# Kernel optimization log

Measured on AMD Instinct MI355X. Metric: run time of the kernel, lower is better.

## Reference

```python
import jax, jax.numpy as jnp
import numpy as np

N = 50000          # num nodes
E = 800000         # num edges (avg degree 16)
IN_C, HID_C, OUT_C = 128, 128, 64
LPA_ITER = 5


def setup_inputs() -> dict:
    key = jax.random.key(0)
    ks = jax.random.split(key, 8)
    x = jax.random.normal(ks[0], (N, IN_C), dtype=jnp.float32)
    soft_labels = jax.random.uniform(ks[1], (N, OUT_C), dtype=jnp.float32)
    edge_index = jax.random.randint(ks[2], (2, E), 0, N, dtype=jnp.int64)
    # learnable edge weights: abs() in the original, so keep them positive
    edge_attr = jax.random.uniform(ks[3], (E,), dtype=jnp.float32, minval=0.1, maxval=1.0)
    # GCNConv params (lin weight + bias)
    w1 = jax.random.normal(ks[4], (IN_C, HID_C), dtype=jnp.float32) / np.sqrt(IN_C)
    b1 = jnp.zeros((HID_C,), dtype=jnp.float32)
    w2 = jax.random.normal(ks[5], (HID_C, OUT_C), dtype=jnp.float32) / np.sqrt(HID_C)
    b2 = jnp.zeros((OUT_C,), dtype=jnp.float32)
    return {"x": x, "soft_labels": soft_labels, "edge_attr": edge_attr,
            "w1": w1, "b1": b1, "w2": w2, "b2": b2, "edge_index": edge_index}


def reference(x, soft_labels, edge_attr, w1, b1, w2, b2, edge_index):
    row, col = edge_index[0], edge_index[1]
    n = x.shape[0]
    # row-normalize the weighted sparse adjacency: A_n = D^{-1} A
    deg = jax.ops.segment_sum(edge_attr, row, num_segments=n)  # [N]
    deg_inv = jnp.where(deg == 0, 0.0, 1.0 / deg)              # inf -> 0
    val = deg_inv[row] * edge_attr                              # [E]

    def spmm(v):  # A_n @ v,  v: [N, F]
        return jax.ops.segment_sum(val[:, None] * v[col], row, num_segments=n)

    # eval mode: dropout(p=0.5, training=False) is identity
    h = jax.nn.relu(spmm(x @ w1) + b1)        # GCNConv 1 (normalize=False)
    logits = spmm(h @ w2) + b2                # GCNConv 2
    x_out = jax.nn.sigmoid(logits)

    labels = soft_labels
    for _ in range(LPA_ITER):                 # label propagation
        labels = spmm(labels)
    labels = jax.nn.sigmoid(labels)
    return (x_out, labels)
```

## Files before the change

kernel.cpp:

```cpp
#include <hip/hip_runtime.h>
#include <cstdint>
#include <cstddef>


#define WS_ALIGN(x) (((x) + 255) & ~((size_t)255))

typedef __attribute__((ext_vector_type(8))) short short8;
typedef __attribute__((ext_vector_type(4))) float floatx4;

__device__ __forceinline__ unsigned short f2bf(float f) {
    unsigned u = __float_as_uint(f);
    u += 0x7fffu + ((u >> 16) & 1u);
    return (unsigned short)(u >> 16);
}
__device__ __forceinline__ float bf2f(unsigned short h) {
    return __uint_as_float(((unsigned)h) << 16);
}
__device__ __forceinline__ float sigmoidf(float x) {
    return 1.f / (1.f + __expf(-x));
}

static const int NBLK = 256;
#define MAXNB 256

__launch_bounds__(256)
__global__ void binA_count(const int* __restrict__ row, int* __restrict__ bucket_count,
                           int* __restrict__ bases, int E, int chunk, int NB)
{
    __shared__ int hist[MAXNB];
    const int t = threadIdx.x;
    const int blk = blockIdx.x;
    if (t < NB) hist[t] = 0;
    __syncthreads();
    const int s = blk * chunk;
    const int e = min(E, s + chunk);
    for (int i = s + t; i < e; i += 256)
        atomicAdd(&hist[row[i] >> 8], 1);
    __syncthreads();
    if (t < NB)
        bases[blk * NB + t] = atomicAdd(&bucket_count[t], hist[t]);
}

__launch_bounds__(256)
__global__ void bin_scan(const int* __restrict__ bucket_count, int* __restrict__ bucket_start,
                         int NB)
{
    __shared__ int s[256];
    const int t = threadIdx.x;
    int v = (t < NB) ? bucket_count[t] : 0;
    s[t] = v;
    __syncthreads();
    for (int off = 1; off < 256; off <<= 1) {
        int u = (t >= off) ? s[t - off] : 0;
        __syncthreads();
        s[t] += u;
        __syncthreads();
    }
    int excl = s[t] - v;
    if (t <= NB) bucket_start[t] = excl;
}

__launch_bounds__(256)
__global__ void binA_scatter(const int* __restrict__ row, const int* __restrict__ colv,
                             const float* __restrict__ ea,
                             const int* __restrict__ bucket_start, const int* __restrict__ bases,
                             int2* __restrict__ bk, int E, int chunk, int NB)
{
    __shared__ int cur[MAXNB];
    const int t = threadIdx.x;
    const int blk = blockIdx.x;
    if (t < NB) cur[t] = bucket_start[t] + bases[blk * NB + t];
    __syncthreads();
    const int s = blk * chunk;
    const int e = min(E, s + chunk);
    for (int i = s + t; i < e; i += 256) {
        int r = row[i];
        int bin = r >> 8;
        int pos = atomicAdd(&cur[bin], 1);
        bk[pos] = make_int2(((r & 255) << 16) | colv[i], __float_as_int(ea[i]));
    }
}

__launch_bounds__(256)
__global__ void binB(const int2* __restrict__ bk, const int* __restrict__ bucket_start,
                     int* __restrict__ rowptr, int2* __restrict__ edges, int N)
{
    __shared__ int cnt[256];
    __shared__ float deg[256];
    __shared__ float inv[256];
    __shared__ int excl_s[256];
    __shared__ int cur[256];
    __shared__ int scantmp[256];
    const int b = blockIdx.x;
    const int t = threadIdx.x;
    const int s = bucket_start[b];
    const int e = bucket_start[b + 1];
    cnt[t] = 0;
    deg[t] = 0.f;
    __syncthreads();
    for (int i = s + t; i < e; i += 256) {
        int2 v = bk[i];
        int rl = ((unsigned)v.x) >> 16;
        atomicAdd(&cnt[rl], 1);
        atomicAdd(&deg[rl], __int_as_float(v.y));
    }
    __syncthreads();
    const int myc = cnt[t];
    scantmp[t] = myc;
    __syncthreads();
    for (int off = 1; off < 256; off <<= 1) {
        int u = (t >= off) ? scantmp[t - off] : 0;
        __syncthreads();
        scantmp[t] += u;
        __syncthreads();
    }
    const int excl = scantmp[t] - myc;
    excl_s[t] = excl;
    float d = deg[t];
    inv[t] = (d > 0.f) ? 1.f / d : 0.f;
    cur[t] = 0;
    const int gr = b * 256 + t;
    if (gr <= N) rowptr[gr] = s + excl;
    __syncthreads();
    for (int i = s + t; i < e; i += 256) {
        int2 v = bk[i];
        int rl = ((unsigned)v.x) >> 16;
        int c = v.x & 0xffff;
        int p = s + excl_s[rl] + atomicAdd(&cur[rl], 1);
        edges[p] = make_int2(c, __float_as_int(__int_as_float(v.y) * inv[rl]));
    }
}

__global__ void f32_to_bf16_kernel(const float* __restrict__ in, unsigned short* __restrict__ out,
                                   int n2)
{
    int i = blockIdx.x * 256 + threadIdx.x;
    if (i < n2) {
        float2 v = ((const float2*)in)[i];
        unsigned p = (unsigned)f2bf(v.x) | ((unsigned)f2bf(v.y) << 16);
        ((unsigned*)out)[i] = p;
    }
}

template<int COLS>
__global__ void pack_w_kernel(const float* __restrict__ W, unsigned short* __restrict__ Wp)
{
    const int total = (COLS / 16) * 4 * 64;
    int idx = blockIdx.x * 256 + threadIdx.x;
    if (idx >= total) return;
    const int l = idx & 63;
    const int t = (idx >> 6) & 3;
    const int ct = idx >> 8;
    const int kbase = t * 32 + (l >> 4) * 8;
    const int col = ct * 16 + (l & 15);
    unsigned short v[8];
#pragma unroll
    for (int j = 0; j < 8; ++j)
        v[j] = f2bf(W[(size_t)(kbase + j) * COLS + col]);
    uint4 o;
    o.x = (unsigned)v[0] | ((unsigned)v[1] << 16);
    o.y = (unsigned)v[2] | ((unsigned)v[3] << 16);
    o.z = (unsigned)v[4] | ((unsigned)v[5] << 16);
    o.w = (unsigned)v[6] | ((unsigned)v[7] << 16);
    *(uint4*)(Wp + (size_t)idx * 8) = o;
}

template<int COLS>
__launch_bounds__(256)
__global__ void gemm_mfma_f32a(const float* __restrict__ A,
                               const unsigned short* __restrict__ Wp,
                               unsigned short* __restrict__ C, int M)
{
    const int wave = threadIdx.x >> 6;
    const int lane = threadIdx.x & 63;
    const int row0 = blockIdx.x * 64 + wave * 16;
    const int m = lane & 15;
    const int q = lane >> 4;

    const int arow = row0 + m;
    const bool avalid = arow < M;
    short8 a[4];
#pragma unroll
    for (int t = 0; t < 4; ++t) {
        if (avalid) {
            float4 f0 = *(const float4*)(A + (size_t)arow * 128 + t * 32 + q * 8);
            float4 f1 = *(const float4*)(A + (size_t)arow * 128 + t * 32 + q * 8 + 4);
            a[t][0] = (short)f2bf(f0.x); a[t][1] = (short)f2bf(f0.y);
            a[t][2] = (short)f2bf(f0.z); a[t][3] = (short)f2bf(f0.w);
            a[t][4] = (short)f2bf(f1.x); a[t][5] = (short)f2bf(f1.y);
            a[t][6] = (short)f2bf(f1.z); a[t][7] = (short)f2bf(f1.w);
        } else {
            a[t] = (short8)0;
        }
    }

#pragma unroll
    for (int ct = 0; ct < COLS / 16; ++ct) {
        floatx4 acc = {0.f, 0.f, 0.f, 0.f};
#pragma unroll
        for (int t = 0; t < 4; ++t) {
            short8 b = *(const short8*)(Wp + (size_t)((ct * 4 + t) * 64 + lane) * 8);
            acc = __builtin_amdgcn_mfma_f32_16x16x32_bf16(a[t], b, acc, 0, 0, 0);
        }
        const int col = ct * 16 + m;
#pragma unroll
        for (int r = 0; r < 4; ++r) {
            int orow = row0 + q * 4 + r;
            if (orow < M)
                C[(size_t)orow * COLS + col] = f2bf(acc[r]);
        }
    }
}

template<int COLS>
__launch_bounds__(256)
__global__ void gemm_mfma(const unsigned short* __restrict__ A,
                          const unsigned short* __restrict__ Wp,
                          unsigned short* __restrict__ C, int M)
{
    const int wave = threadIdx.x >> 6;
    const int lane = threadIdx.x & 63;
    const int row0 = blockIdx.x * 64 + wave * 16;
    const int m = lane & 15;
    const int q = lane >> 4;

    const int arow = row0 + m;
    const bool avalid = arow < M;
    short8 a[4];
#pragma unroll
    for (int t = 0; t < 4; ++t) {
        if (avalid)
            a[t] = *(const short8*)(A + (size_t)arow * 128 + t * 32 + q * 8);
        else
            a[t] = (short8)0;
    }

#pragma unroll
    for (int ct = 0; ct < COLS / 16; ++ct) {
        floatx4 acc = {0.f, 0.f, 0.f, 0.f};
#pragma unroll
        for (int t = 0; t < 4; ++t) {
            short8 b = *(const short8*)(Wp + (size_t)((ct * 4 + t) * 64 + lane) * 8);
            acc = __builtin_amdgcn_mfma_f32_16x16x32_bf16(a[t], b, acc, 0, 0, 0);
        }
        const int col = ct * 16 + m;
#pragma unroll
        for (int r = 0; r < 4; ++r) {
            int orow = row0 + q * 4 + r;
            if (orow < M)
                C[(size_t)orow * COLS + col] = f2bf(acc[r]);
        }
    }
}

__launch_bounds__(256)
__global__ void spmm_f128_f64(const int* __restrict__ rowptr, const int2* __restrict__ edges,
                              const unsigned* __restrict__ srcA,
                              const unsigned short* __restrict__ srcB,
                              const float* __restrict__ bias,
                              unsigned* __restrict__ outA,
                              unsigned short* __restrict__ outB,
                              int n)
{
    const int row = blockIdx.x * 4 + (threadIdx.x >> 6);
    const int lane = threadIdx.x & 63;
    if (row >= n) return;
    const int s = rowptr[row];
    const int e = rowptr[row + 1];

    float ax[8], ay[8], ab[8];
#pragma unroll
    for (int j = 0; j < 8; ++j) { ax[j] = 0.f; ay[j] = 0.f; ab[j] = 0.f; }
    int i = s;
    for (; i + 8 <= e; i += 8) {
        int2 ed[8];
        unsigned ua[8];
        unsigned short ub[8];
#pragma unroll
        for (int j = 0; j < 8; ++j) ed[j] = edges[i + j];
#pragma unroll
        for (int j = 0; j < 8; ++j) ua[j] = srcA[(size_t)ed[j].x * 64 + lane];
#pragma unroll
        for (int j = 0; j < 8; ++j) ub[j] = srcB[(size_t)ed[j].x * 64 + lane];
#pragma unroll
        for (int j = 0; j < 8; ++j) {
            float w = __int_as_float(ed[j].y);
            ax[j] = fmaf(w, __uint_as_float(ua[j] << 16), ax[j]);
            ay[j] = fmaf(w, __uint_as_float(ua[j] & 0xffff0000u), ay[j]);
            ab[j] = fmaf(w, bf2f(ub[j]), ab[j]);
        }
    }
    for (; i < e; ++i) {
        int2 e0 = edges[i];
        unsigned ua = srcA[(size_t)e0.x * 64 + lane];
        unsigned short ub = srcB[(size_t)e0.x * 64 + lane];
        float w = __int_as_float(e0.y);
        ax[0] = fmaf(w, __uint_as_float(ua << 16), ax[0]);
        ay[0] = fmaf(w, __uint_as_float(ua & 0xffff0000u), ay[0]);
        ab[0] = fmaf(w, bf2f(ub), ab[0]);
    }
    float vx = ((ax[0] + ax[1]) + (ax[2] + ax[3])) + ((ax[4] + ax[5]) + (ax[6] + ax[7]));
    float vy = ((ay[0] + ay[1]) + (ay[2] + ay[3])) + ((ay[4] + ay[5]) + (ay[6] + ay[7]));
    float vb = ((ab[0] + ab[1]) + (ab[2] + ab[3])) + ((ab[4] + ab[5]) + (ab[6] + ab[7]));
    float2 b = *(const float2*)(bias + lane * 2);
    vx = fmaxf(vx + b.x, 0.f);
    vy = fmaxf(vy + b.y, 0.f);
    outA[(size_t)row * 64 + lane] = (unsigned)f2bf(vx) | ((unsigned)f2bf(vy) << 16);
    outB[(size_t)row * 64 + lane] = f2bf(vb);
}

__launch_bounds__(256)
__global__ void spmm_f64_f64(const int* __restrict__ rowptr, const int2* __restrict__ edges,
                             const unsigned short* __restrict__ srcA,
                             const unsigned short* __restrict__ srcB,
                             const float* __restrict__ bias,
                             float* __restrict__ outA,
                             unsigned short* __restrict__ outB,
                             int n)
{
    const int row = blockIdx.x * 4 + (threadIdx.x >> 6);
    const int lane = threadIdx.x & 63;
    if (row >= n) return;
    const int s = rowptr[row];
    const int e = rowptr[row + 1];

    float aa[8], ab[8];
#pragma unroll
    for (int j = 0; j < 8; ++j) { aa[j] = 0.f; ab[j] = 0.f; }
    int i = s;
    for (; i + 8 <= e; i += 8) {
        int2 ed[8];
        unsigned short ua[8], ub[8];
#pragma unroll
        for (int j = 0; j < 8; ++j) ed[j] = edges[i + j];
#pragma unroll
        for (int j = 0; j < 8; ++j) ua[j] = srcA[(size_t)ed[j].x * 64 + lane];
#pragma unroll
        for (int j = 0; j < 8; ++j) ub[j] = srcB[(size_t)ed[j].x * 64 + lane];
#pragma unroll
        for (int j = 0; j < 8; ++j) {
            float w = __int_as_float(ed[j].y);
            aa[j] = fmaf(w, bf2f(ua[j]), aa[j]);
            ab[j] = fmaf(w, bf2f(ub[j]), ab[j]);
        }
    }
    for (; i < e; ++i) {
        int2 e0 = edges[i];
        float w = __int_as_float(e0.y);
        aa[0] = fmaf(w, bf2f(srcA[(size_t)e0.x * 64 + lane]), aa[0]);
        ab[0] = fmaf(w, bf2f(srcB[(size_t)e0.x * 64 + lane]), ab[0]);
    }
    float va = ((aa[0] + aa[1]) + (aa[2] + aa[3])) + ((aa[4] + aa[5]) + (aa[6] + aa[7]));
    float vb = ((ab[0] + ab[1]) + (ab[2] + ab[3])) + ((ab[4] + ab[5]) + (ab[6] + ab[7]));
    outA[(size_t)row * 64 + lane] = sigmoidf(va + bias[lane]);
    outB[(size_t)row * 64 + lane] = f2bf(vb);
}

template<int ACT, bool OUT_BF16>
__launch_bounds__(256)
__global__ void spmm64_kernel(const int* __restrict__ rowptr, const int2* __restrict__ edges,
                              const unsigned short* __restrict__ src,
                              void* __restrict__ out, int n)
{
    const int row = blockIdx.x * 4 + (threadIdx.x >> 6);
    const int lane = threadIdx.x & 63;
    if (row >= n) return;
    const int s = rowptr[row];
    const int e = rowptr[row + 1];

    float a[8];
#pragma unroll
    for (int j = 0; j < 8; ++j) a[j] = 0.f;
    int i = s;
    for (; i + 8 <= e; i += 8) {
        int2 ed[8];
        float sv[8];
#pragma unroll
        for (int j = 0; j < 8; ++j) ed[j] = edges[i + j];
#pragma unroll
        for (int j = 0; j < 8; ++j) sv[j] = bf2f(src[(size_t)ed[j].x * 64 + lane]);
#pragma unroll
        for (int j = 0; j < 8; ++j) a[j] = fmaf(__int_as_float(ed[j].y), sv[j], a[j]);
    }
    for (; i < e; ++i) {
        int2 e0 = edges[i];
        a[0] = fmaf(__int_as_float(e0.y), bf2f(src[(size_t)e0.x * 64 + lane]), a[0]);
    }
    float v = ((a[0] + a[1]) + (a[2] + a[3])) + ((a[4] + a[5]) + (a[6] + a[7]));
    if (ACT == 3) v = sigmoidf(v);
    if (OUT_BF16)
        ((unsigned short*)out)[(size_t)row * 64 + lane] = f2bf(v);
    else
        ((float*)out)[(size_t)row * 64 + lane] = v;
}

extern "C" void kernel_launch(void* const* d_in, const int* in_sizes, int n_in,
                              void* d_out, int out_size, void* d_ws, size_t ws_size,
                              hipStream_t stream)
{
    const float* x    = (const float*)d_in[0];
    const float* soft = (const float*)d_in[1];
    const float* ea   = (const float*)d_in[2];
    const float* w1   = (const float*)d_in[3];
    const float* b1   = (const float*)d_in[4];
    const float* w2   = (const float*)d_in[5];
    const float* b2   = (const float*)d_in[6];
    const int*   eidx = (const int*)d_in[7];

    const int N = in_sizes[0] / 128;
    const int E = in_sizes[2];
    const int* row  = eidx;
    const int* colv = eidx + E;
    const int NB = (N + 255) / 256;
    const int chunk = (E + NBLK - 1) / NBLK;

    uint8_t* ws = (uint8_t*)d_ws;
    size_t off = 0;
    auto alloc = [&](size_t bytes) -> void* {
        void* p = ws + off;
        off += WS_ALIGN(bytes);
        return p;
    };
    int*  bucket_count = (int*) alloc((size_t)NB * 4);
    int*  bucket_start = (int*) alloc(((size_t)NB + 1) * 4);
    int*  bases        = (int*) alloc((size_t)NBLK * NB * 4);
    int*  rowptr       = (int*) alloc(((size_t)N + 1) * 4);
    int2* bk           = (int2*)alloc((size_t)E * 8);
    int2* edges        = (int2*)alloc((size_t)E * 8);
    unsigned short* w1p     = (unsigned short*)alloc((size_t)128 * 128 * 2);
    unsigned short* w2p     = (unsigned short*)alloc((size_t)128 * 64 * 2);
    unsigned short* xw1b    = (unsigned short*)alloc((size_t)N * 128 * 2);
    unsigned short* hb      = (unsigned short*)alloc((size_t)N * 128 * 2);
    unsigned short* logitsb = (unsigned short*)alloc((size_t)N * 64 * 2);
    unsigned short* softb   = (unsigned short*)alloc((size_t)N * 64 * 2);
    unsigned short* labA    = (unsigned short*)alloc((size_t)N * 64 * 2);
    unsigned short* labB    = (unsigned short*)alloc((size_t)N * 64 * 2);

    float* out0 = (float*)d_out;
    float* out1 = out0 + (size_t)N * 64;

    hipMemsetAsync(bucket_count, 0, (size_t)NB * 4, stream);

    binA_count<<<NBLK, 256, 0, stream>>>(row, bucket_count, bases, E, chunk, NB);
    bin_scan<<<1, 256, 0, stream>>>(bucket_count, bucket_start, NB);
    binA_scatter<<<NBLK, 256, 0, stream>>>(row, colv, ea, bucket_start, bases, bk, E, chunk, NB);
    binB<<<NB, 256, 0, stream>>>(bk, bucket_start, rowptr, edges, N);

    const int ns2 = (N * 64) / 2;
    f32_to_bf16_kernel<<<(ns2 + 255) / 256, 256, 0, stream>>>(soft, softb, ns2);
    pack_w_kernel<128><<<8, 256, 0, stream>>>(w1, w1p);
    pack_w_kernel<64><<<4, 256, 0, stream>>>(w2, w2p);

    const int gGemm = (N + 63) / 64;
    const int gSp   = (N + 3) / 4;

    gemm_mfma_f32a<128><<<gGemm, 256, 0, stream>>>(x, w1p, xw1b, N);

    spmm_f128_f64<<<gSp, 256, 0, stream>>>(rowptr, edges, (const unsigned*)xw1b, softb,
                                           b1, (unsigned*)hb, labA, N);

    gemm_mfma<64><<<gGemm, 256, 0, stream>>>(hb, w2p, logitsb, N);

    spmm_f64_f64<<<gSp, 256, 0, stream>>>(rowptr, edges, logitsb, labA, b2, out0, labB, N);

    spmm64_kernel<0, true ><<<gSp, 256, 0, stream>>>(rowptr, edges, labB, labA, N);
    spmm64_kernel<0, true ><<<gSp, 256, 0, stream>>>(rowptr, edges, labA, labB, N);
    spmm64_kernel<3, false><<<gSp, 256, 0, stream>>>(rowptr, edges, labB, out1, N);
}
```

Baseline: 361.9 us.

## Split each SpMM row across four edge-quarters with vectorized bf16 gathers, merge small kernels

The SpMM kernels now assign each wave's four 16-lane quarters to different edges. Each lane gathers a vector (uint2/uint4) of packed bf16 features, and the partial sums are combined with cross-lane shuffles at the end. Edge records are read with nontemporal loads. The bucket scan is folded into the scatter and binB kernels, and the weight and label conversions are merged into one prep kernel, which removes several launches. This widens memory transactions and increases edge-level parallelism, at the cost of redundant scans per block and idle lanes on low-degree rows.

```diff
diff --git a/kernel.cpp b/kernel.cpp
--- a/kernel.cpp
+++ b/kernel.cpp
@@ -13,11 +13,20 @@
     u += 0x7fffu + ((u >> 16) & 1u);
     return (unsigned short)(u >> 16);
 }
-__device__ __forceinline__ float bf2f(unsigned short h) {
-    return __uint_as_float(((unsigned)h) << 16);
+__device__ __forceinline__ float bf_lo(unsigned u) { return __uint_as_float(u << 16); }
+__device__ __forceinline__ float bf_hi(unsigned u) { return __uint_as_float(u & 0xffff0000u); }
+__device__ __forceinline__ unsigned pack_bf2(float a, float b) {
+    return (unsigned)f2bf(a) | ((unsigned)f2bf(b) << 16);
 }
 __device__ __forceinline__ float sigmoidf(float x) {
     return 1.f / (1.f + __expf(-x));
+}
+__device__ __forceinline__ int2 ld_nt_int2(const int2* p) {
+    long long v = __builtin_nontemporal_load((const long long*)p);
+    int2 r;
+    r.x = (int)(unsigned)(v & 0xffffffffLL);
+    r.y = (int)(v >> 32);
+    return r;
 }
 
 static const int NBLK = 256;
@@ -42,34 +51,25 @@
 }
 
 __launch_bounds__(256)
-__global__ void bin_scan(const int* __restrict__ bucket_count, int* __restrict__ bucket_start,
-                         int NB)
-{
-    __shared__ int s[256];
-    const int t = threadIdx.x;
-    int v = (t < NB) ? bucket_count[t] : 0;
-    s[t] = v;
-    __syncthreads();
-    for (int off = 1; off < 256; off <<= 1) {
-        int u = (t >= off) ? s[t - off] : 0;
-        __syncthreads();
-        s[t] += u;
-        __syncthreads();
-    }
-    int excl = s[t] - v;
-    if (t <= NB) bucket_start[t] = excl;
-}
-
-__launch_bounds__(256)
 __global__ void binA_scatter(const int* __restrict__ row, const int* __restrict__ colv,
                              const float* __restrict__ ea,
-                             const int* __restrict__ bucket_start, const int* __restrict__ bases,
+                             const int* __restrict__ bucket_count, const int* __restrict__ bases,
                              int2* __restrict__ bk, int E, int chunk, int NB)
 {
+    __shared__ int scan[256];
     __shared__ int cur[MAXNB];
     const int t = threadIdx.x;
     const int blk = blockIdx.x;
-    if (t < NB) cur[t] = bucket_start[t] + bases[blk * NB + t];
+    int v = (t < NB) ? bucket_count[t] : 0;
+    scan[t] = v;
+    __syncthreads();
+    for (int off = 1; off < 256; off <<= 1) {
+        int u = (t >= off) ? scan[t - off] : 0;
+        __syncthreads();
+        scan[t] += u;
+        __syncthreads();
+    }
+    if (t < NB) cur[t] = (scan[t] - v) + bases[blk * NB + t];
     __syncthreads();
     const int s = blk * chunk;
     const int e = min(E, s + chunk);
@@ -82,27 +82,39 @@
 }
 
 __launch_bounds__(256)
-__global__ void binB(const int2* __restrict__ bk, const int* __restrict__ bucket_start,
-                     int* __restrict__ rowptr, int2* __restrict__ edges, int N)
-{
+__global__ void binB(const int2* __restrict__ bk, const int* __restrict__ bucket_count,
+                     int* __restrict__ rowptr, int2* __restrict__ edges, int N, int NB)
+{
+    __shared__ int scan[256];
     __shared__ int cnt[256];
     __shared__ float deg[256];
     __shared__ float inv[256];
     __shared__ int excl_s[256];
     __shared__ int cur[256];
     __shared__ int scantmp[256];
+    __shared__ int sse[2];
     const int b = blockIdx.x;
     const int t = threadIdx.x;
-    const int s = bucket_start[b];
-    const int e = bucket_start[b + 1];
+    int v = (t < NB) ? bucket_count[t] : 0;
+    scan[t] = v;
+    __syncthreads();
+    for (int off = 1; off < 256; off <<= 1) {
+        int u = (t >= off) ? scan[t - off] : 0;
+        __syncthreads();
+        scan[t] += u;
+        __syncthreads();
+    }
+    if (t == b) { sse[0] = scan[t] - v; sse[1] = scan[t]; }
     cnt[t] = 0;
     deg[t] = 0.f;
     __syncthreads();
+    const int s = sse[0];
+    const int e = sse[1];
     for (int i = s + t; i < e; i += 256) {
-        int2 v = bk[i];
-        int rl = ((unsigned)v.x) >> 16;
+        int2 w = bk[i];
+        int rl = ((unsigned)w.x) >> 16;
         atomicAdd(&cnt[rl], 1);
-        atomicAdd(&deg[rl], __int_as_float(v.y));
+        atomicAdd(&deg[rl], __int_as_float(w.y));
     }
     __syncthreads();
     const int myc = cnt[t];
@@ -123,31 +135,18 @@
     if (gr <= N) rowptr[gr] = s + excl;
     __syncthreads();
     for (int i = s + t; i < e; i += 256) {
-        int2 v = bk[i];
-        int rl = ((unsigned)v.x) >> 16;
-        int c = v.x & 0xffff;
+        int2 w = bk[i];
+        int rl = ((unsigned)w.x) >> 16;
+        int c = w.x & 0xffff;
         int p = s + excl_s[rl] + atomicAdd(&cur[rl], 1);
-        edges[p] = make_int2(c, __float_as_int(__int_as_float(v.y) * inv[rl]));
-    }
-}
-
-__global__ void f32_to_bf16_kernel(const float* __restrict__ in, unsigned short* __restrict__ out,
-                                   int n2)
-{
-    int i = blockIdx.x * 256 + threadIdx.x;
-    if (i < n2) {
-        float2 v = ((const float2*)in)[i];
-        unsigned p = (unsigned)f2bf(v.x) | ((unsigned)f2bf(v.y) << 16);
-        ((unsigned*)out)[i] = p;
-    }
-}
-
-template<int COLS>
-__global__ void pack_w_kernel(const float* __restrict__ W, unsigned short* __restrict__ Wp)
-{
-    const int total = (COLS / 16) * 4 * 64;
-    int idx = blockIdx.x * 256 + threadIdx.x;
-    if (idx >= total) return;
+        edges[p] = make_int2(c, __float_as_int(__int_as_float(w.y) * inv[rl]));
+    }
+}
+
+__device__ __forceinline__ void pack_w_elem(const float* __restrict__ W,
+                                            unsigned short* __restrict__ Wp,
+                                            int idx, int COLS)
+{
     const int l = idx & 63;
     const int t = (idx >> 6) & 3;
     const int ct = idx >> 8;
@@ -163,6 +162,27 @@
     o.z = (unsigned)v[4] | ((unsigned)v[5] << 16);
     o.w = (unsigned)v[6] | ((unsigned)v[7] << 16);
     *(uint4*)(Wp + (size_t)idx * 8) = o;
+}
+
+__launch_bounds__(256)
+__global__ void prep_kernel(const float* __restrict__ w1, const float* __restrict__ w2,
+                            const float* __restrict__ soft,
+                            unsigned short* __restrict__ w1p, unsigned short* __restrict__ w2p,
+                            unsigned short* __restrict__ softb, int ns2)
+{
+    const int blk = blockIdx.x;
+    const int t = threadIdx.x;
+    if (blk < 8) {
+        pack_w_elem(w1, w1p, blk * 256 + t, 128);
+    } else if (blk < 12) {
+        pack_w_elem(w2, w2p, (blk - 8) * 256 + t, 64);
+    } else {
+        int i = (blk - 12) * 256 + t;
+        if (i < ns2) {
+            float2 v = ((const float2*)soft)[i];
+            ((unsigned*)softb)[i] = pack_bf2(v.x, v.y);
+        }
+    }
 }
 
 template<int COLS>
@@ -254,144 +274,246 @@
 }
 
 __launch_bounds__(256)
-__global__ void spmm_f128_f64(const int* __restrict__ rowptr, const int2* __restrict__ edges,
-                              const unsigned* __restrict__ srcA,
-                              const unsigned short* __restrict__ srcB,
-                              const float* __restrict__ bias,
-                              unsigned* __restrict__ outA,
-                              unsigned short* __restrict__ outB,
-                              int n)
+__global__ void fused1_quad(const int* __restrict__ rowptr, const int2* __restrict__ edges,
+                            const uint4* __restrict__ srcA,
+                            const uint2* __restrict__ srcB,
+                            const float* __restrict__ bias,
+                            uint4* __restrict__ outA,
+                            uint2* __restrict__ outB,
+                            int n)
 {
     const int row = blockIdx.x * 4 + (threadIdx.x >> 6);
     const int lane = threadIdx.x & 63;
+    const int fl = lane & 15;
+    const int q = lane >> 4;
     if (row >= n) return;
     const int s = rowptr[row];
     const int e = rowptr[row + 1];
 
-    float ax[8], ay[8], ab[8];
-#pragma unroll
-    for (int j = 0; j < 8; ++j) { ax[j] = 0.f; ay[j] = 0.f; ab[j] = 0.f; }
+    float ax[8], as[4];
+#pragma unroll
+    for (int j = 0; j < 8; ++j) ax[j] = 0.f;
+#pragma unroll
+    for (int j = 0; j < 4; ++j) as[j] = 0.f;
+
     int i = s;
-    for (; i + 8 <= e; i += 8) {
-        int2 ed[8];
-        unsigned ua[8];
-        unsigned short ub[8];
-#pragma unroll
-        for (int j = 0; j < 8; ++j) ed[j] = edges[i + j];
-#pragma unroll
-        for (int j = 0; j < 8; ++j) ua[j] = srcA[(size_t)ed[j].x * 64 + lane];
-#pragma unroll
-        for (int j = 0; j < 8; ++j) ub[j] = srcB[(size_t)ed[j].x * 64 + lane];
-#pragma unroll
-        for (int j = 0; j < 8; ++j) {
+    for (; i + 16 <= e; i += 16) {
+        int2 ed[4]; uint4 ua[4]; uint2 ub[4];
+#pragma unroll
+        for (int j = 0; j < 4; ++j) ed[j] = ld_nt_int2(&edges[i + 4 * j + q]);
+#pragma unroll
+        for (int j = 0; j < 4; ++j) ua[j] = srcA[(size_t)ed[j].x * 16 + fl];
+#pragma unroll
+        for (int j = 0; j < 4; ++j) ub[j] = srcB[(size_t)ed[j].x * 16 + fl];
+#pragma unroll
+        for (int j = 0; j < 4; ++j) {
             float w = __int_as_float(ed[j].y);
-            ax[j] = fmaf(w, __uint_as_float(ua[j] << 16), ax[j]);
-            ay[j] = fmaf(w, __uint_as_float(ua[j] & 0xffff0000u), ay[j]);
-            ab[j] = fmaf(w, bf2f(ub[j]), ab[j]);
-        }
-    }
-    for (; i < e; ++i) {
-        int2 e0 = edges[i];
-        unsigned ua = srcA[(size_t)e0.x * 64 + lane];
-        unsigned short ub = srcB[(size_t)e0.x * 64 + lane];
-        float w = __int_as_float(e0.y);
-        ax[0] = fmaf(w, __uint_as_float(ua << 16), ax[0]);
-        ay[0] = fmaf(w, __uint_as_float(ua & 0xffff0000u), ay[0]);
-        ab[0] = fmaf(w, bf2f(ub), ab[0]);
-    }
-    float vx = ((ax[0] + ax[1]) + (ax[2] + ax[3])) + ((ax[4] + ax[5]) + (ax[6] + ax[7]));
-    float vy = ((ay[0] + ay[1]) + (ay[2] + ay[3])) + ((ay[4] + ay[5]) + (ay[6] + ay[7]));
-    float vb = ((ab[0] + ab[1]) + (ab[2] + ab[3])) + ((ab[4] + ab[5]) + (ab[6] + ab[7]));
-    float2 b = *(const float2*)(bias + lane * 2);
-    vx = fmaxf(vx + b.x, 0.f);
-    vy = fmaxf(vy + b.y, 0.f);
-    outA[(size_t)row * 64 + lane] = (unsigned)f2bf(vx) | ((unsigned)f2bf(vy) << 16);
-    outB[(size_t)row * 64 + lane] = f2bf(vb);
-}
-
-__launch_bounds__(256)
-__global__ void spmm_f64_f64(const int* __restrict__ rowptr, const int2* __restrict__ edges,
-                             const unsigned short* __restrict__ srcA,
-                             const unsigned short* __restrict__ srcB,
-                             const float* __restrict__ bias,
-                             float* __restrict__ outA,
-                             unsigned short* __restrict__ outB,
-                             int n)
+            ax[0] = fmaf(w, bf_lo(ua[j].x), ax[0]); ax[1] = fmaf(w, bf_hi(ua[j].x), ax[1]);
+            ax[2] = fmaf(w, bf_lo(ua[j].y), ax[2]); ax[3] = fmaf(w, bf_hi(ua[j].y), ax[3]);
+            ax[4] = fmaf(w, bf_lo(ua[j].z), ax[4]); ax[5] = fmaf(w, bf_hi(ua[j].z), ax[5]);
+            ax[6] = fmaf(w, bf_lo(ua[j].w), ax[6]); ax[7] = fmaf(w, bf_hi(ua[j].w), ax[7]);
+            as[0] = fmaf(w, bf_lo(ub[j].x), as[0]); as[1] = fmaf(w, bf_hi(ub[j].x), as[1]);
+            as[2] = fmaf(w, bf_lo(ub[j].y), as[2]); as[3] = fmaf(w, bf_hi(ub[j].y), as[3]);
+        }
+    }
+    for (; i + 4 <= e; i += 4) {
+        int2 ed = ld_nt_int2(&edges[i + q]);
+        uint4 ua = srcA[(size_t)ed.x * 16 + fl];
+        uint2 ub = srcB[(size_t)ed.x * 16 + fl];
+        float w = __int_as_float(ed.y);
+        ax[0] = fmaf(w, bf_lo(ua.x), ax[0]); ax[1] = fmaf(w, bf_hi(ua.x), ax[1]);
+        ax[2] = fmaf(w, bf_lo(ua.y), ax[2]); ax[3] = fmaf(w, bf_hi(ua.y), ax[3]);
+        ax[4] = fmaf(w, bf_lo(ua.z), ax[4]); ax[5] = fmaf(w, bf_hi(ua.z), ax[5]);
+        ax[6] = fmaf(w, bf_lo(ua.w), ax[6]); ax[7] = fmaf(w, bf_hi(ua.w), ax[7]);
+        as[0] = fmaf(w, bf_lo(ub.x), as[0]); as[1] = fmaf(w, bf_hi(ub.x), as[1]);
+        as[2] = fmaf(w, bf_lo(ub.y), as[2]); as[3] = fmaf(w, bf_hi(ub.y), as[3]);
+    }
+    const int r = e - i;
+    if (q < r) {
+        int2 ed = ld_nt_int2(&edges[i + q]);
+        uint4 ua = srcA[(size_t)ed.x * 16 + fl];
+        uint2 ub = srcB[(size_t)ed.x * 16 + fl];
+        float w = __int_as_float(ed.y);
+        ax[0] = fmaf(w, bf_lo(ua.x), ax[0]); ax[1] = fmaf(w, bf_hi(ua.x), ax[1]);
+        ax[2] = fmaf(w, bf_lo(ua.y), ax[2]); ax[3] = fmaf(w, bf_hi(ua.y), ax[3]);
+        ax[4] = fmaf(w, bf_lo(ua.z), ax[4]); ax[5] = fmaf(w, bf_hi(ua.z), ax[5]);
+        ax[6] = fmaf(w, bf_lo(ua.w), ax[6]); ax[7] = fmaf(w, bf_hi(ua.w), ax[7]);
+        as[0] = fmaf(w, bf_lo(ub.x), as[0]); as[1] = fmaf(w, bf_hi(ub.x), as[1]);
+        as[2] = fmaf(w, bf_lo(ub.y), as[2]); as[3] = fmaf(w, bf_hi(ub.y), as[3]);
+    }
+#pragma unroll
+    for (int j = 0; j < 8; ++j) {
+        ax[j] += __shfl_down(ax[j], 32);
+        ax[j] += __shfl_down(ax[j], 16);
+    }
+#pragma unroll
+    for (int j = 0; j < 4; ++j) {
+        as[j] += __shfl_down(as[j], 32);
+        as[j] += __shfl_down(as[j], 16);
+    }
+    if (q == 0) {
+        float4 b0 = *(const float4*)(bias + 8 * fl);
+        float4 b1 = *(const float4*)(bias + 8 * fl + 4);
+        float h0 = fmaxf(ax[0] + b0.x, 0.f), h1 = fmaxf(ax[1] + b0.y, 0.f);
+        float h2 = fmaxf(ax[2] + b0.z, 0.f), h3 = fmaxf(ax[3] + b0.w, 0.f);
+        float h4 = fmaxf(ax[4] + b1.x, 0.f), h5 = fmaxf(ax[5] + b1.y, 0.f);
+        float h6 = fmaxf(ax[6] + b1.z, 0.f), h7 = fmaxf(ax[7] + b1.w, 0.f);
+        uint4 oa;
+        oa.x = pack_bf2(h0, h1); oa.y = pack_bf2(h2, h3);
+        oa.z = pack_bf2(h4, h5); oa.w = pack_bf2(h6, h7);
+        outA[(size_t)row * 16 + fl] = oa;
+        uint2 ob;
+        ob.x = pack_bf2(as[0], as[1]);
+        ob.y = pack_bf2(as[2], as[3]);
+        outB[(size_t)row * 16 + fl] = ob;
+    }
+}
+
+__launch_bounds__(256)
+__global__ void fused2_quad(const int* __restrict__ rowptr, const int2* __restrict__ edges,
+                            const uint2* __restrict__ srcA,
+                            const uint2* __restrict__ srcB,
+                            const float* __restrict__ bias,
+                            float* __restrict__ outA,
+                            uint2* __restrict__ outB,
+                            int n)
 {
     const int row = blockIdx.x * 4 + (threadIdx.x >> 6);
     const int lane = threadIdx.x & 63;
+    const int fl = lane & 15;
+    const int q = lane >> 4;
     if (row >= n) return;
     const int s = rowptr[row];
     const int e = rowptr[row + 1];
 
-    float aa[8], ab[8];
-#pragma unroll
-    for (int j = 0; j < 8; ++j) { aa[j] = 0.f; ab[j] = 0.f; }
+    float aa[4], ab[4];
+#pragma unroll
+    for (int j = 0; j < 4; ++j) { aa[j] = 0.f; ab[j] = 0.f; }
+
     int i = s;
-    for (; i + 8 <= e; i += 8) {
-        int2 ed[8];
-        unsigned short ua[8], ub[8];
-#pragma unroll
-        for (int j = 0; j < 8; ++j) ed[j] = edges[i + j];
-#pragma unroll
-        for (int j = 0; j < 8; ++j) ua[j] = srcA[(size_t)ed[j].x * 64 + lane];
-#pragma unroll
-        for (int j = 0; j < 8; ++j) ub[j] = srcB[(size_t)ed[j].x * 64 + lane];
-#pragma unroll
-        for (int j = 0; j < 8; ++j) {
+    for (; i + 16 <= e; i += 16) {
+        int2 ed[4]; uint2 ua[4], ub[4];
+#pragma unroll
+        for (int j = 0; j < 4; ++j) ed[j] = ld_nt_int2(&edges[i + 4 * j + q]);
+#pragma unroll
+        for (int j = 0; j < 4; ++j) ua[j] = srcA[(size_t)ed[j].x * 16 + fl];
+#pragma unroll
+        for (int j = 0; j < 4; ++j) ub[j] = srcB[(size_t)ed[j].x * 16 + fl];
+#pragma unroll
+        for (int j = 0; j < 4; ++j) {
             float w = __int_as_float(ed[j].y);
-            aa[j] = fmaf(w, bf2f(ua[j]), aa[j]);
-            ab[j] = fmaf(w, bf2f(ub[j]), ab[j]);
-        }
-    }
-    for (; i < e; ++i) {
-        int2 e0 = edges[i];
-        float w = __int_as_float(e0.y);
-        aa[0] = fmaf(w, bf2f(srcA[(size_t)e0.x * 64 + lane]), aa[0]);
-        ab[0] = fmaf(w, bf2f(srcB[(size_t)e0.x * 64 + lane]), ab[0]);
-    }
-    float va = ((aa[0] + aa[1]) + (aa[2] + aa[3])) + ((aa[4] + aa[5]) + (aa[6] + aa[7]));
-    float vb = ((ab[0] + ab[1]) + (ab[2] + ab[3])) + ((ab[4] + ab[5]) + (ab[6] + ab[7]));
-    outA[(size_t)row * 64 + lane] = sigmoidf(va + bias[lane]);
-    outB[(size_t)row * 64 + lane] = f2bf(vb);
-}
-
-template<int ACT, bool OUT_BF16>
-__launch_bounds__(256)
-__global__ void spmm64_kernel(const int* __restrict__ rowptr, const int2* __restrict__ edges,
-                              const unsigned short* __restrict__ src,
-                              void* __restrict__ out, int n)
+            aa[0] = fmaf(w, bf_lo(ua[j].x), aa[0]); aa[1] = fmaf(w, bf_hi(ua[j].x), aa[1]);
+            aa[2] = fmaf(w, bf_lo(ua[j].y), aa[2]); aa[3] = fmaf(w, bf_hi(ua[j].y), aa[3]);
+            ab[0] = fmaf(w, bf_lo(ub[j].x), ab[0]); ab[1] = fmaf(w, bf_hi(ub[j].x), ab[1]);
+            ab[2] = fmaf(w, bf_lo(ub[j].y), ab[2]); ab[3] = fmaf(w, bf_hi(ub[j].y), ab[3]);
+        }
+    }
+    for (; i + 4 <= e; i += 4) {
+        int2 ed = ld_nt_int2(&edges[i + q]);
+        uint2 ua = srcA[(size_t)ed.x * 16 + fl];
+        uint2 ub = srcB[(size_t)ed.x * 16 + fl];
+        float w = __int_as_float(ed.y);
+        aa[0] = fmaf(w, bf_lo(ua.x), aa[0]); aa[1] = fmaf(w, bf_hi(ua.x), aa[1]);
+        aa[2] = fmaf(w, bf_lo(ua.y), aa[2]); aa[3] = fmaf(w, bf_hi(ua.y), aa[3]);
+        ab[0] = fmaf(w, bf_lo(ub.x), ab[0]); ab[1] = fmaf(w, bf_hi(ub.x), ab[1]);
+        ab[2] = fmaf(w, bf_lo(ub.y), ab[2]); ab[3] = fmaf(w, bf_hi(ub.y), ab[3]);
+    }
+    const int r = e - i;
+    if (q < r) {
+        int2 ed = ld_nt_int2(&edges[i + q]);
+        uint2 ua = srcA[(size_t)ed.x * 16 + fl];
+        uint2 ub = srcB[(size_t)ed.x * 16 + fl];
+        float w = __int_as_float(ed.y);
+        aa[0] = fmaf(w, bf_lo(ua.x), aa[0]); aa[1] = fmaf(w, bf_hi(ua.x), aa[1]);
+        aa[2] = fmaf(w, bf_lo(ua.y), aa[2]); aa[3] = fmaf(w, bf_hi(ua.y), aa[3]);
+        ab[0] = fmaf(w, bf_lo(ub.x), ab[0]); ab[1] = fmaf(w, bf_hi(ub.x), ab[1]);
+        ab[2] = fmaf(w, bf_lo(ub.y), ab[2]); ab[3] = fmaf(w, bf_hi(ub.y), ab[3]);
+    }
+#pragma unroll
+    for (int j = 0; j < 4; ++j) {
+        aa[j] += __shfl_down(aa[j], 32); aa[j] += __shfl_down(aa[j], 16);
+        ab[j] += __shfl_down(ab[j], 32); ab[j] += __shfl_down(ab[j], 16);
+    }
+    if (q == 0) {
+        float4 bb = *(const float4*)(bias + 4 * fl);
+        float4 o;
+        o.x = sigmoidf(aa[0] + bb.x);
+        o.y = sigmoidf(aa[1] + bb.y);
+        o.z = sigmoidf(aa[2] + bb.z);
+        o.w = sigmoidf(aa[3] + bb.w);
+        *(float4*)(outA + (size_t)row * 64 + 4 * fl) = o;
+        uint2 ob;
+        ob.x = pack_bf2(ab[0], ab[1]);
+        ob.y = pack_bf2(ab[2], ab[3]);
+        outB[(size_t)row * 16 + fl] = ob;
+    }
+}
+
+template<int ACT>
+__launch_bounds__(256)
+__global__ void spmm64_quad(const int* __restrict__ rowptr, const int2* __restrict__ edges,
+                            const uint2* __restrict__ src,
+                            void* __restrict__ out, int n)
 {
     const int row = blockIdx.x * 4 + (threadIdx.x >> 6);
     const int lane = threadIdx.x & 63;
+    const int fl = lane & 15;
+    const int q = lane >> 4;
     if (row >= n) return;
     const int s = rowptr[row];
     const int e = rowptr[row + 1];
 
-    float a[8];
-#pragma unroll
-    for (int j = 0; j < 8; ++j) a[j] = 0.f;
+    float a[4];
+#pragma unroll
+    for (int j = 0; j < 4; ++j) a[j] = 0.f;
+
     int i = s;
-    for (; i + 8 <= e; i += 8) {
-        int2 ed[8];
-        float sv[8];
-#pragma unroll
-        for (int j = 0; j < 8; ++j) ed[j] = edges[i + j];
-#pragma unroll
-        for (int j = 0; j < 8; ++j) sv[j] = bf2f(src[(size_t)ed[j].x * 64 + lane]);
-#pragma unroll
-        for (int j = 0; j < 8; ++j) a[j] = fmaf(__int_as_float(ed[j].y), sv[j], a[j]);
-    }
-    for (; i < e; ++i) {
-        int2 e0 = edges[i];
-        a[0] = fmaf(__int_as_float(e0.y), bf2f(src[(size_t)e0.x * 64 + lane]), a[0]);
-    }
-    float v = ((a[0] + a[1]) + (a[2] + a[3])) + ((a[4] + a[5]) + (a[6] + a[7]));
-    if (ACT == 3) v = sigmoidf(v);
-    if (OUT_BF16)
-        ((unsigned short*)out)[(size_t)row * 64 + lane] = f2bf(v);
-    else
-        ((float*)out)[(size_t)row * 64 + lane] = v;
+    for (; i + 16 <= e; i += 16) {
+        int2 ed[4]; uint2 u[4];
+#pragma unroll
+        for (int j = 0; j < 4; ++j) ed[j] = ld_nt_int2(&edges[i + 4 * j + q]);
+#pragma unroll
+        for (int j = 0; j < 4; ++j) u[j] = src[(size_t)ed[j].x * 16 + fl];
+#pragma unroll
+        for (int j = 0; j < 4; ++j) {
+            float w = __int_as_float(ed[j].y);
+            a[0] = fmaf(w, bf_lo(u[j].x), a[0]); a[1] = fmaf(w, bf_hi(u[j].x), a[1]);
+            a[2] = fmaf(w, bf_lo(u[j].y), a[2]); a[3] = fmaf(w, bf_hi(u[j].y), a[3]);
+        }
+    }
+    for (; i + 4 <= e; i += 4) {
+        int2 ed = ld_nt_int2(&edges[i + q]);
+        uint2 u = src[(size_t)ed.x * 16 + fl];
+        float w = __int_as_float(ed.y);
+        a[0] = fmaf(w, bf_lo(u.x), a[0]); a[1] = fmaf(w, bf_hi(u.x), a[1]);
+        a[2] = fmaf(w, bf_lo(u.y), a[2]); a[3] = fmaf(w, bf_hi(u.y), a[3]);
+    }
+    const int r = e - i;
+    if (q < r) {
+        int2 ed = ld_nt_int2(&edges[i + q]);
+        uint2 u = src[(size_t)ed.x * 16 + fl];
+        float w = __int_as_float(ed.y);
+        a[0] = fmaf(w, bf_lo(u.x), a[0]); a[1] = fmaf(w, bf_hi(u.x), a[1]);
+        a[2] = fmaf(w, bf_lo(u.y), a[2]); a[3] = fmaf(w, bf_hi(u.y), a[3]);
+    }
+#pragma unroll
+    for (int j = 0; j < 4; ++j) {
+        a[j] += __shfl_down(a[j], 32);
+        a[j] += __shfl_down(a[j], 16);
+    }
+    if (q == 0) {
+        if (ACT == 0) {
+            uint2 o;
+            o.x = pack_bf2(a[0], a[1]);
+            o.y = pack_bf2(a[2], a[3]);
+            ((uint2*)out)[(size_t)row * 16 + fl] = o;
+        } else {
+            float4 o;
+            o.x = sigmoidf(a[0]); o.y = sigmoidf(a[1]);
+            o.z = sigmoidf(a[2]); o.w = sigmoidf(a[3]);
+            *(float4*)((float*)out + (size_t)row * 64 + 4 * fl) = o;
+        }
+    }
 }
 
 extern "C" void kernel_launch(void* const* d_in, const int* in_sizes, int n_in,
@@ -422,7 +544,6 @@
         return p;
     };
     int*  bucket_count = (int*) alloc((size_t)NB * 4);
-    int*  bucket_start = (int*) alloc(((size_t)NB + 1) * 4);
     int*  bases        = (int*) alloc((size_t)NBLK * NB * 4);
     int*  rowptr       = (int*) alloc(((size_t)N + 1) * 4);
     int2* bk           = (int2*)alloc((size_t)E * 8);
@@ -442,28 +563,28 @@
     hipMemsetAsync(bucket_count, 0, (size_t)NB * 4, stream);
 
     binA_count<<<NBLK, 256, 0, stream>>>(row, bucket_count, bases, E, chunk, NB);
-    bin_scan<<<1, 256, 0, stream>>>(bucket_count, bucket_start, NB);
-    binA_scatter<<<NBLK, 256, 0, stream>>>(row, colv, ea, bucket_start, bases, bk, E, chunk, NB);
-    binB<<<NB, 256, 0, stream>>>(bk, bucket_start, rowptr, edges, N);
+    binA_scatter<<<NBLK, 256, 0, stream>>>(row, colv, ea, bucket_count, bases, bk, E, chunk, NB);
+    binB<<<NB, 256, 0, stream>>>(bk, bucket_count, rowptr, edges, N, NB);
 
     const int ns2 = (N * 64) / 2;
-    f32_to_bf16_kernel<<<(ns2 + 255) / 256, 256, 0, stream>>>(soft, softb, ns2);
-    pack_w_kernel<128><<<8, 256, 0, stream>>>(w1, w1p);
-    pack_w_kernel<64><<<4, 256, 0, stream>>>(w2, w2p);
+    prep_kernel<<<12 + (ns2 + 255) / 256, 256, 0, stream>>>(w1, w2, soft, w1p, w2p, softb, ns2);
 
     const int gGemm = (N + 63) / 64;
     const int gSp   = (N + 3) / 4;
 
     gemm_mfma_f32a<128><<<gGemm, 256, 0, stream>>>(x, w1p, xw1b, N);
 
-    spmm_f128_f64<<<gSp, 256, 0, stream>>>(rowptr, edges, (const unsigned*)xw1b, softb,
-                                           b1, (unsigned*)hb, labA, N);
+    fused1_quad<<<gSp, 256, 0, stream>>>(rowptr, edges, (const uint4*)xw1b,
+                                         (const uint2*)softb, b1,
+                                         (uint4*)hb, (uint2*)labA, N);
 
     gemm_mfma<64><<<gGemm, 256, 0, stream>>>(hb, w2p, logitsb, N);
 
-    spmm_f64_f64<<<gSp, 256, 0, stream>>>(rowptr, edges, logitsb, labA, b2, out0, labB, N);
-
-    spmm64_kernel<0, true ><<<gSp, 256, 0, stream>>>(rowptr, edges, labB, labA, N);
-    spmm64_kernel<0, true ><<<gSp, 256, 0, stream>>>(rowptr, edges, labA, labB, N);
-    spmm64_kernel<3, false><<<gSp, 256, 0, stream>>>(rowptr, edges, labB, out1, N);
-}
+    fused2_quad<<<gSp, 256, 0, stream>>>(rowptr, edges, (const uint2*)logitsb,
+                                         (const uint2*)labA, b2,
+                                         out0, (uint2*)labB, N);
+
+    spmm64_quad<0><<<gSp, 256, 0, stream>>>(rowptr, edges, (const uint2*)labB, labA, N);
+    spmm64_quad<0><<<gSp, 256, 0, stream>>>(rowptr, edges, (const uint2*)labA, labB, N);
+    spmm64_quad<3><<<gSp, 256, 0, stream>>>(rowptr, edges, (const uint2*)labB, out1, N);
+}
```

Result: faster. 318.2 us (-12.1%).
